# Kernel optimization log

Measured on AMD Instinct MI355X. Metric: run time of the kernel, lower is better.

## Reference

```python
import jax, jax.numpy as jnp
import numpy as np

# ---- module config (init_kwargs) ----
B, CIN, H, W_ = 2, 64, 56, 56
COUT, KH, KW = 128, 3, 3
K = CIN * KH * KW               # 576, reduction dim
ARRAY_ROWS = 128
IN_SLICES = (2, 2, 2, 2)        # 8-bit inputs, 2-bit slices
W_SLICES = (2, 2, 2, 2)         # 8-bit weights, 2-bit slices
N_STEPS_IN = 2 ** sum(IN_SLICES)    # 256, unsigned quantizer
N_STEPS_W = 2 ** sum(W_SLICES)      # 256
ADC_BINS = 256
ADC_STEP = 4.0

def _shifts_masks(slices):
    masks, shifts = [], [0]
    for s in slices[::-1]:
        masks.append((1 << s) - 1)
        shifts.append(s + shifts[-1])
    return np.array(shifts[-2::-1], np.int32), np.array(masks[::-1], np.int32)

_ish, _im = _shifts_masks(IN_SLICES)
_wsh, _wm = _shifts_masks(W_SLICES)
ISH, IM = jnp.asarray(_ish), jnp.asarray(_im)
WSH, WM = jnp.asarray(_wsh), jnp.asarray(_wm)
ISF = jnp.asarray((1 << _ish).astype(np.float32))  # slice recombine weights 2^shift
WSF = jnp.asarray((1 << _wsh).astype(np.float32))


def setup_inputs() -> dict:
    key = jax.random.key(0)
    k1, k2 = jax.random.split(key)
    return {
        "x": jax.random.normal(k1, (B, CIN, H, W_), jnp.float32),
        "w": jax.random.normal(k2, (COUT, CIN, KH, KW), jnp.float32),
    }


def _im2col(x):
    # 3x3 SAME conv patches, ordering [Cin, kh, kw] to match w.reshape(COUT, K)
    xp = jnp.pad(x, ((0, 0), (0, 0), (1, 1), (1, 1)))
    cols = jnp.stack([xp[:, :, i:i + H, j:j + W_]
                      for i in range(KH) for j in range(KW)], axis=2)  # [B,Cin,9,H,W]
    return cols.transpose(0, 3, 4, 1, 2).reshape(B * H * W_, K)  # [Nx, K]


def _quant_unsigned(v, n_steps):
    # Quantizer.offset + Quantizer.forward (unsigned, per-row over dim=-1)
    offs = v.min(axis=-1, keepdims=True)
    vr = v - offs
    step = vr.max(axis=-1, keepdims=True) / (n_steps - 1)
    q = jnp.round(jnp.clip(vr, 0.0, step * n_steps) / step).astype(jnp.int32)
    return q, step[..., 0], offs[..., 0]


def _slice_bits(q, shifts, masks):
    # Slicer.forward: stack (q >> shift) & mask along new leading slice dim
    s = shifts.reshape((-1,) + (1,) * q.ndim)
    m = masks.reshape((-1,) + (1,) * q.ndim)
    return (q[None] >> s) & m


def _chunk(t):
    # Chunker.forward over last dim K
    nb = -(-K // ARRAY_ROWS)
    npb = -(-K // nb)
    pad = nb * npb - K
    t = jnp.pad(t, [(0, 0)] * (t.ndim - 1) + [(0, pad)])
    t = t.reshape(t.shape[:-1] + (nb, npb))
    return jnp.moveaxis(t, -2, 0)  # [nb, ..., npb]


def reference(x, w):
    xf = _im2col(x)                    # [Nx, K]
    wf = w.reshape(COUT, K)            # [Ny, K]
    x_sum = xf.sum(axis=-1)            # [Nx]
    w_sum = wf.sum(axis=-1)            # [Ny]

    xq, x_scale, x_offs = _quant_unsigned(xf, N_STEPS_IN)
    wq, w_scale, w_offs = _quant_unsigned(wf, N_STEPS_W)

    xc = _chunk(_slice_bits(xq, ISH, IM))  # [nb, nis, Nx, npb] int32
    wc = _chunk(_slice_bits(wq, WSH, WM))  # [nb, nws, Ny, npb] int32

    # bit-serial crossbar MACs per (chunk, weight-slice, input-slice)
    z = jnp.einsum('bixk,bwyk->bwixy',
                   xc.astype(jnp.float32), wc.astype(jnp.float32))  # [nb,nws,nis,Nx,Ny]

    # ADC digitization (unsigned, fixed step): quantize then dequantize
    z = jnp.round(jnp.clip(z, 0.0, ADC_STEP * ADC_BINS) / ADC_STEP) * ADC_STEP

    # Chunker.reverse: sum crossbar blocks; Slicer.reverse: shift-weighted sums
    z = z.sum(axis=0)                               # [nws,nis,Nx,Ny]
    z = jnp.einsum('wixy,w,i->xy', z, WSF, ISF)     # [Nx,Ny]

    # dequantize scales and unsigned-offset correction:
    # x.y = sx*sy*(xq.yq) + x_offs*sum(y) + y_offs*sum(x) - x_offs*y_offs*K
    z = z * x_scale[:, None] * w_scale[None, :]
    z = (z + x_offs[:, None] * w_sum[None, :]
           + w_offs[None, :] * x_sum[:, None]
           - x_offs[:, None] * w_offs[None, :] * K)

    return z.reshape(B, H, W_, COUT).transpose(0, 3, 1, 2)  # [B,Cout,H,W]
```

## Files before the change

### kernel.cpp

```cpp
#include <hip/hip_runtime.h>


#define KDIM  576
#define NPB   116
#define SSTR  688

typedef int i32x4 __attribute__((ext_vector_type(4)));
typedef float f32x4 __attribute__((ext_vector_type(4)));

__device__ __forceinline__ i32x4 slice2b(i32x4 v, int sh) {
    i32x4 r;
    r[0] = (int)(((unsigned)v[0] >> sh) & 0x03030303u);
    r[1] = (int)(((unsigned)v[1] >> sh) & 0x03030303u);
    r[2] = (int)(((unsigned)v[2] >> sh) & 0x03030303u);
    r[3] = (int)(((unsigned)v[3] >> sh) & 0x03030303u);
    return r;
}

__device__ __forceinline__ void quant36(const float (&v)[36], unsigned char* rowp,
                                        int i16, float* sc, float* of,
                                        float* sm_, int sidx)
{
    float mn = v[0], mx = v[0], sm = 0.f;
#pragma unroll
    for (int m = 0; m < 36; m++) { mn = fminf(mn, v[m]); mx = fmaxf(mx, v[m]); sm += v[m]; }
#pragma unroll
    for (int off = 1; off < 16; off <<= 1) {
        mn = fminf(mn, __shfl_xor(mn, off));
        mx = fmaxf(mx, __shfl_xor(mx, off));
        sm += __shfl_xor(sm, off);
    }
    float step = (mx - mn) / 255.0f;
    if (i16 == 0) { sc[sidx] = step; of[sidx] = mn; sm_[sidx] = sm; }
    int k0 = i16 * 36;
#pragma unroll
    for (int d = 0; d < 9; d++) {
        unsigned int dw = 0;
#pragma unroll
        for (int mb = 0; mb < 4; mb++) {
            int q = (int)rintf((v[d * 4 + mb] - mn) / step);
            q = q < 0 ? 0 : (q > 255 ? 255 : q);
            dw |= (unsigned)q << (8 * mb);
        }
        int kd = k0 + d * 4;
        int ch = kd / NPB;
        *(unsigned int*)(rowp + kd + 12 * ch) = dw;
    }
}

__device__ __forceinline__ void zero_pad_row(unsigned char* scr, int idx) {
    int rl = idx >> 4, dwp = idx & 15;
    int col = dwp < 12 ? (dwp / 3) * 128 + 116 + (dwp % 3) * 4
                       : 624 + (dwp - 12) * 4;
    *(unsigned int*)(scr + rl * SSTR + col) = 0u;
}

__device__ __forceinline__ void copy_out(const unsigned char* scr,
                                         unsigned char* dst, int tid) {
    for (int idx = tid; idx < 640; idx += 256) {
        int u = idx >> 4, rl = idx & 15;
        int dst16 = (u >> 3) * 128 + ((u >> 2) & 1) * 64 + (u & 3) * 16 + rl;
        *(i32x4*)(dst + dst16 * 16) = *(const i32x4*)(scr + rl * SSTR + u * 16);
    }
}

__global__ __launch_bounds__(256) void k_q(
    const float* __restrict__ x, const float* __restrict__ w,
    unsigned char* __restrict__ Xq, unsigned char* __restrict__ Wq,
    float* __restrict__ xscg, float* __restrict__ xofg, float* __restrict__ xsmg,
    float* __restrict__ wscg, float* __restrict__ wofg, float* __restrict__ wsmg)
{
    __shared__ float xs2[64 * 57];
    __shared__ __align__(16) unsigned char scr[16 * SSTR];

    int tid = threadIdx.x, wv = tid >> 6, lane = tid & 63;
    int g = lane >> 4, i16 = lane & 15;
    int blk = blockIdx.x;

    if (blk < 392) {
        int b = blk >= 196 ? 1 : 0;
        int pos0 = (blk - 196 * b) * 16;
        const float* xb = x + (size_t)(b * 64) * 3136;
        for (int i = tid; i < 64 * 54; i += 256) {
            int cin = i / 54, rem = i - cin * 54;
            int kh = rem / 18;
            int gg = pos0 + (rem - kh * 18) - 1;
            float vv = 0.f;
            if (gg >= 0 && gg < 3136) {
                int hg = gg / 56, wg = gg - hg * 56;
                int r = hg - 1 + kh;
                if (r >= 0 && r < 56) vv = xb[cin * 3136 + r * 56 + wg];
            }
            xs2[cin * 57 + rem] = vv;
        }
        zero_pad_row(scr, tid);
        __syncthreads();

        int i = wv * 4 + g;
        int pos = pos0 + i;
        int w_ = pos - (pos / 56) * 56;
        float v[36];
#pragma unroll
        for (int m = 0; m < 36; m++) {
            int r9 = m % 9, kh = r9 / 3, kw = r9 - kh * 3;
            int cin = i16 * 4 + m / 9;
            int ww = w_ - 1 + kw;
            v[m] = (ww >= 0 && ww < 56) ? xs2[cin * 57 + kh * 18 + i + kw] : 0.f;
        }
        quant36(v, scr + i * SSTR, i16, xscg, xofg, xsmg, blk * 16 + i);
        __syncthreads();

        copy_out(scr, Xq + (size_t)blk * 10240, tid);
    } else {
        int ctile = blk - 392;
        zero_pad_row(scr, tid);
        int rl = wv * 4 + g;
        int row = ctile * 16 + rl;
        const float* wr = w + (size_t)row * KDIM + i16 * 36;
        float v[36];
#pragma unroll
        for (int d = 0; d < 9; d++) {
            f32x4 t = *(const f32x4*)(wr + d * 4);
            v[d*4+0] = t[0]; v[d*4+1] = t[1]; v[d*4+2] = t[2]; v[d*4+3] = t[3];
        }
        quant36(v, scr + rl * SSTR, i16, wscg, wofg, wsmg, row);
        __syncthreads();

        copy_out(scr, Wq + (size_t)ctile * 10240, tid);
    }
}

__device__ __forceinline__ void chunk_ws(const unsigned char* xt, const unsigned char* wt,
                                         int ch, int lane, i32x4 (&acc4)[4])
{
    const i32x4 zero = {0, 0, 0, 0};
    i32x4 x0 = *(const i32x4*)(xt + ch * 2048 + lane * 16);
    i32x4 x1 = *(const i32x4*)(xt + ch * 2048 + 1024 + lane * 16);
    i32x4 w0 = *(const i32x4*)(wt + ch * 2048 + lane * 16);
    i32x4 w1 = *(const i32x4*)(wt + ch * 2048 + 1024 + lane * 16);
    i32x4 ws0[4], ws1[4];
#pragma unroll
    for (int ws = 0; ws < 4; ws++) {
        ws0[ws] = slice2b(w0, 6 - 2 * ws);
        ws1[ws] = slice2b(w1, 6 - 2 * ws);
    }
#pragma unroll
    for (int is = 0; is < 4; is++) {
        int ish = 6 - 2 * is;
        i32x4 a0 = slice2b(x0, ish), a1 = slice2b(x1, ish);
#pragma unroll
        for (int ws = 0; ws < 4; ws++) {
            i32x4 d = __builtin_amdgcn_mfma_i32_16x16x64_i8(ws0[ws], a0, zero, 0, 0, 0);
            d = __builtin_amdgcn_mfma_i32_16x16x64_i8(ws1[ws], a1, d, 0, 0, 0);
            int sh = ish + 6 - 2 * ws;
#pragma unroll
            for (int r = 0; r < 4; r++) {
                int z = d[r];
                z = z > 1024 ? 1024 : z;
                int t = (z >> 2) & 1;
                int r4 = (z + 1 + t) & ~3;
                acc4[ws][r] += r4 << sh;
            }
        }
    }
}

__global__ __launch_bounds__(256) void k_d(
    const unsigned char* __restrict__ Xq, const unsigned char* __restrict__ Wq,
    const float* __restrict__ xscg, const float* __restrict__ xofg,
    const float* __restrict__ xsmg,
    const float* __restrict__ wscg, const float* __restrict__ wofg,
    const float* __restrict__ wsmg, float* __restrict__ out)
{
    __shared__ __align__(16) int pacc[2][64][4];

    int tid = threadIdx.x, wv = tid >> 6, lane = tid & 63;
    int g = lane >> 4, i16 = lane & 15;
    int blk = blockIdx.x;
    int ct = blk & 7, rp = blk >> 3;
    int tl = wv & 1, khalf = wv >> 1;
    int rtile = rp * 2 + tl;
    const unsigned char* xt = Xq + (size_t)rtile * 10240;
    const unsigned char* wt = Wq + (size_t)ct * 10240;

    i32x4 acc4[4] = {{0,0,0,0},{0,0,0,0},{0,0,0,0},{0,0,0,0}};
    if (khalf == 0) {
        chunk_ws(xt, wt, 0, lane, acc4);
        chunk_ws(xt, wt, 1, lane, acc4);
        chunk_ws(xt, wt, 2, lane, acc4);
    } else {
        chunk_ws(xt, wt, 3, lane, acc4);
        chunk_ws(xt, wt, 4, lane, acc4);
    }
    i32x4 acc;
#pragma unroll
    for (int r = 0; r < 4; r++)
        acc[r] = (acc4[0][r] + acc4[1][r]) + (acc4[2][r] + acc4[3][r]);

    if (khalf == 0) *(i32x4*)&pacc[tl][lane][0] = acc;
    __syncthreads();

    if (khalf == 1) {
        i32x4 p = *(const i32x4*)&pacc[tl][lane][0];
#pragma unroll
        for (int r = 0; r < 4; r++) acc[r] += p[r];

        int b = rtile >= 196 ? 1 : 0;
        int xrow = rtile * 16 + i16;
        float xs_ = xscg[xrow], xo = xofg[xrow], xsv = xsmg[xrow];
        int hw = (rtile - 196 * b) * 16 + i16;
#pragma unroll
        for (int r = 0; r < 4; r++) {
            int wrow = ct * 16 + g * 4 + r;
            float tt = ((float)acc[r] * xs_) * wscg[wrow];
            float res = ((tt + xo * wsmg[wrow]) + wofg[wrow] * xsv)
                      - (xo * wofg[wrow]) * 576.0f;
            out[(size_t)(b * 128 + wrow) * 3136 + hw] = res;
        }
    }
}

extern "C" void kernel_launch(void* const* d_in, const int* in_sizes, int n_in,
                              void* d_out, int out_size, void* d_ws, size_t ws_size,
                              hipStream_t stream) {
    const float* x = (const float*)d_in[0];
    const float* w = (const float*)d_in[1];
    float* out = (float*)d_out;

    unsigned char* Xq = (unsigned char*)d_ws;
    unsigned char* Wq = Xq + (size_t)392 * 10240;
    float* xsc = (float*)(Wq + 8 * 10240);
    float* xof = xsc + 6272;
    float* xsm = xof + 6272;
    float* wsc = xsm + 6272;
    float* wof = wsc + 128;
    float* wsm = wof + 128;

    hipLaunchKernelGGL(k_q, dim3(400), dim3(256), 0, stream,
                       x, w, Xq, Wq, xsc, xof, xsm, wsc, wof, wsm);
    hipLaunchKernelGGL(k_d, dim3(1568), dim3(256), 0, stream,
                       Xq, Wq, xsc, xof, xsm, wsc, wof, wsm, out);
}
```

Baseline: 37.12 us.

## Split dot kernel work by input-slice halves and gather quant inputs directly

The MFMA kernel now splits work between wave pairs by input bit-slice (two slices each across all five chunks) instead of by K-chunks (3 vs 2). This balances MFMA counts between the two waves, at the cost of each wave loading all chunk data. The quantization kernel drops the shared-memory staging of input patches and its barrier, reading the 3x3 neighbourhoods straight from global memory. That removes LDS traffic and a sync but adds redundant, less coalesced global loads.

```diff
diff --git a/kernel.cpp b/kernel.cpp
--- a/kernel.cpp
+++ b/kernel.cpp
@@ -70,42 +70,38 @@
     float* __restrict__ xscg, float* __restrict__ xofg, float* __restrict__ xsmg,
     float* __restrict__ wscg, float* __restrict__ wofg, float* __restrict__ wsmg)
 {
-    __shared__ float xs2[64 * 57];
     __shared__ __align__(16) unsigned char scr[16 * SSTR];
 
     int tid = threadIdx.x, wv = tid >> 6, lane = tid & 63;
     int g = lane >> 4, i16 = lane & 15;
     int blk = blockIdx.x;
+
+    zero_pad_row(scr, tid);
 
     if (blk < 392) {
         int b = blk >= 196 ? 1 : 0;
         int pos0 = (blk - 196 * b) * 16;
         const float* xb = x + (size_t)(b * 64) * 3136;
-        for (int i = tid; i < 64 * 54; i += 256) {
-            int cin = i / 54, rem = i - cin * 54;
-            int kh = rem / 18;
-            int gg = pos0 + (rem - kh * 18) - 1;
-            float vv = 0.f;
-            if (gg >= 0 && gg < 3136) {
-                int hg = gg / 56, wg = gg - hg * 56;
-                int r = hg - 1 + kh;
-                if (r >= 0 && r < 56) vv = xb[cin * 3136 + r * 56 + wg];
-            }
-            xs2[cin * 57 + rem] = vv;
-        }
-        zero_pad_row(scr, tid);
-        __syncthreads();
 
         int i = wv * 4 + g;
         int pos = pos0 + i;
-        int w_ = pos - (pos / 56) * 56;
+        int hg = pos / 56, wg = pos - hg * 56;
+
         float v[36];
 #pragma unroll
-        for (int m = 0; m < 36; m++) {
-            int r9 = m % 9, kh = r9 / 3, kw = r9 - kh * 3;
-            int cin = i16 * 4 + m / 9;
-            int ww = w_ - 1 + kw;
-            v[m] = (ww >= 0 && ww < 56) ? xs2[cin * 57 + kh * 18 + i + kw] : 0.f;
+        for (int j = 0; j < 4; j++) {
+            const float* cb = xb + (size_t)(i16 * 4 + j) * 3136;
+#pragma unroll
+            for (int kh = 0; kh < 3; kh++) {
+                int r = hg - 1 + kh;
+                bool rok = (r >= 0 && r < 56);
+#pragma unroll
+                for (int kw = 0; kw < 3; kw++) {
+                    int c = wg - 1 + kw;
+                    bool ok = rok && c >= 0 && c < 56;
+                    v[j * 9 + kh * 3 + kw] = ok ? cb[r * 56 + c] : 0.f;
+                }
+            }
         }
         quant36(v, scr + i * SSTR, i16, xscg, xofg, xsmg, blk * 16 + i);
         __syncthreads();
@@ -113,7 +109,6 @@
         copy_out(scr, Xq + (size_t)blk * 10240, tid);
     } else {
         int ctile = blk - 392;
-        zero_pad_row(scr, tid);
         int rl = wv * 4 + g;
         int row = ctile * 16 + rl;
         const float* wr = w + (size_t)row * KDIM + i16 * 36;
@@ -127,41 +122,6 @@
         __syncthreads();
 
         copy_out(scr, Wq + (size_t)ctile * 10240, tid);
-    }
-}
-
-__device__ __forceinline__ void chunk_ws(const unsigned char* xt, const unsigned char* wt,
-                                         int ch, int lane, i32x4 (&acc4)[4])
-{
-    const i32x4 zero = {0, 0, 0, 0};
-    i32x4 x0 = *(const i32x4*)(xt + ch * 2048 + lane * 16);
-    i32x4 x1 = *(const i32x4*)(xt + ch * 2048 + 1024 + lane * 16);
-    i32x4 w0 = *(const i32x4*)(wt + ch * 2048 + lane * 16);
-    i32x4 w1 = *(const i32x4*)(wt + ch * 2048 + 1024 + lane * 16);
-    i32x4 ws0[4], ws1[4];
-#pragma unroll
-    for (int ws = 0; ws < 4; ws++) {
-        ws0[ws] = slice2b(w0, 6 - 2 * ws);
-        ws1[ws] = slice2b(w1, 6 - 2 * ws);
-    }
-#pragma unroll
-    for (int is = 0; is < 4; is++) {
-        int ish = 6 - 2 * is;
-        i32x4 a0 = slice2b(x0, ish), a1 = slice2b(x1, ish);
-#pragma unroll
-        for (int ws = 0; ws < 4; ws++) {
-            i32x4 d = __builtin_amdgcn_mfma_i32_16x16x64_i8(ws0[ws], a0, zero, 0, 0, 0);
-            d = __builtin_amdgcn_mfma_i32_16x16x64_i8(ws1[ws], a1, d, 0, 0, 0);
-            int sh = ish + 6 - 2 * ws;
-#pragma unroll
-            for (int r = 0; r < 4; r++) {
-                int z = d[r];
-                z = z > 1024 ? 1024 : z;
-                int t = (z >> 2) & 1;
-                int r4 = (z + 1 + t) & ~3;
-                acc4[ws][r] += r4 << sh;
-            }
-        }
     }
 }
 
@@ -178,29 +138,59 @@
     int g = lane >> 4, i16 = lane & 15;
     int blk = blockIdx.x;
     int ct = blk & 7, rp = blk >> 3;
-    int tl = wv & 1, khalf = wv >> 1;
+    int tl = wv & 1, ihalf = wv >> 1;
     int rtile = rp * 2 + tl;
-    const unsigned char* xt = Xq + (size_t)rtile * 10240;
-    const unsigned char* wt = Wq + (size_t)ct * 10240;
-
+    const unsigned char* xt = Xq + (size_t)rtile * 10240 + lane * 16;
+    const unsigned char* wt = Wq + (size_t)ct * 10240 + lane * 16;
+
+    const i32x4 zero = {0, 0, 0, 0};
     i32x4 acc4[4] = {{0,0,0,0},{0,0,0,0},{0,0,0,0},{0,0,0,0}};
-    if (khalf == 0) {
-        chunk_ws(xt, wt, 0, lane, acc4);
-        chunk_ws(xt, wt, 1, lane, acc4);
-        chunk_ws(xt, wt, 2, lane, acc4);
-    } else {
-        chunk_ws(xt, wt, 3, lane, acc4);
-        chunk_ws(xt, wt, 4, lane, acc4);
-    }
+    int is0 = ihalf * 2;
+    int ishA = 6 - 2 * is0;
+    int ishB = ishA - 2;
+
+#pragma unroll
+    for (int ch = 0; ch < 5; ch++) {
+        const unsigned char* xc = xt + ch * 2048;
+        const unsigned char* wc = wt + ch * 2048;
+        i32x4 x0 = *(const i32x4*)(xc), x1 = *(const i32x4*)(xc + 1024);
+        i32x4 w0 = *(const i32x4*)(wc), w1 = *(const i32x4*)(wc + 1024);
+        i32x4 ws0[4], ws1[4];
+#pragma unroll
+        for (int ws = 0; ws < 4; ws++) {
+            ws0[ws] = slice2b(w0, 6 - 2 * ws);
+            ws1[ws] = slice2b(w1, 6 - 2 * ws);
+        }
+#pragma unroll
+        for (int ii = 0; ii < 2; ii++) {
+            int ish = ii ? ishB : ishA;
+            i32x4 a0 = slice2b(x0, ish), a1 = slice2b(x1, ish);
+#pragma unroll
+            for (int ws = 0; ws < 4; ws++) {
+                i32x4 d = __builtin_amdgcn_mfma_i32_16x16x64_i8(ws0[ws], a0, zero, 0, 0, 0);
+                d = __builtin_amdgcn_mfma_i32_16x16x64_i8(ws1[ws], a1, d, 0, 0, 0);
+                int sh = ish + 6 - 2 * ws;
+#pragma unroll
+                for (int r = 0; r < 4; r++) {
+                    int z = d[r];
+                    z = z > 1024 ? 1024 : z;
+                    int t = (z >> 2) & 1;
+                    int r4 = (z + 1 + t) & ~3;
+                    acc4[ws][r] += r4 << sh;
+                }
+            }
+        }
+    }
+
     i32x4 acc;
 #pragma unroll
     for (int r = 0; r < 4; r++)
         acc[r] = (acc4[0][r] + acc4[1][r]) + (acc4[2][r] + acc4[3][r]);
 
-    if (khalf == 0) *(i32x4*)&pacc[tl][lane][0] = acc;
+    if (ihalf == 0) *(i32x4*)&pacc[tl][lane][0] = acc;
     __syncthreads();
 
-    if (khalf == 1) {
+    if (ihalf == 1) {
         i32x4 p = *(const i32x4*)&pacc[tl][lane][0];
 #pragma unroll
         for (int r = 0; r < 4; r++) acc[r] += p[r];
```

Result: slower. 38.89 us (+4.8%).
